# Kernel tuning notes

Measured on AMD Instinct MI355X. Metric: run time of the kernel, lower is better.

## Reference

```python
import jax, jax.numpy as jnp
import numpy as np

L, B, T = 512, 256, 128  # seq_length, batch_size, num_tags


def setup_inputs() -> dict:
    key = jax.random.key(0)
    k0, k1, k2, k3, k4 = jax.random.split(key, 5)
    emissions = jax.random.normal(k0, (L, B, T), dtype=jnp.float32)
    tags = jax.random.randint(k1, (L, B), 0, T)
    mask = jnp.ones((L, B), dtype=jnp.int32)
    # params per reset_parameters: uniform(-0.1, 0.1)
    start_transitions = jax.random.uniform(k2, (T,), jnp.float32, -0.1, 0.1)
    end_transitions = jax.random.uniform(k3, (T,), jnp.float32, -0.1, 0.1)
    transitions = jax.random.uniform(k4, (T, T), jnp.float32, -0.1, 0.1)
    return {
        'emissions': emissions,
        'tags': tags,
        'mask': mask,
        'start_transitions': start_transitions,
        'end_transitions': end_transitions,
        'transitions': transitions,
    }


def _compute_score(emissions, tags, maskf, start_transitions, end_transitions, transitions):
    # emissions: (L,B,T), tags/maskf: (L,B)
    # emission score at the gold tag for every (masked) position. The original
    # loop adds emissions[i][tags[i]]*mask[i] for i<L-1 and the last valid
    # position's emission via the end term; with 0/1 mask this equals the
    # full masked sum (padded positions contribute 0, last valid position is
    # counted exactly once either way).
    em_score = jnp.take_along_axis(emissions, tags[..., None], axis=2)[..., 0]  # (L,B)
    score = start_transitions[tags[0]] + jnp.sum(em_score * maskf, axis=0)  # (B,)
    # transition score between consecutive gold tags, masked by next position
    tr = transitions[tags[:-1], tags[1:]]  # (L-1,B)
    score = score + jnp.sum(tr * maskf[1:], axis=0)
    # end transition from the last valid tag of each sequence
    last_idx = jnp.sum(maskf, axis=0).astype(jnp.int32) - 1  # (B,)
    last_tags = jnp.take_along_axis(tags, last_idx[None, :], axis=0)[0]  # (B,)
    score = score + end_transitions[last_tags]
    return score


def _compute_normalizer(emissions, maskf, start_transitions, end_transitions, transitions):
    # forward algorithm: logsumexp recursion over timesteps via lax.scan
    def step(log_prob, xs):
        em, m = xs  # em: (B,T), m: (B,)
        # (B,T_prev,1) + (1,T_prev,T_next) + (B,1,T_next) -> logsumexp over prev
        score = jax.nn.logsumexp(
            log_prob[:, :, None] + transitions[None, :, :] + em[:, None, :], axis=1)
        log_prob = score * m[:, None] + log_prob * (1.0 - m[:, None])
        return log_prob, None

    lp0 = start_transitions[None, :] + emissions[0]  # (B,T)
    lp, _ = jax.lax.scan(jax.checkpoint(step), lp0, (emissions[1:], maskf[1:]))
    return jax.nn.logsumexp(lp + end_transitions[None, :], axis=1)  # (B,)


def reference(emissions, tags, mask, start_transitions, end_transitions, transitions):
    maskf = mask.astype(emissions.dtype)
    numerator = _compute_score(emissions, tags, maskf, start_transitions,
                               end_transitions, transitions)
    denominator = _compute_normalizer(emissions, maskf, start_transitions,
                                      end_transitions, transitions)
    llh = numerator - denominator  # (B,)
    return jnp.sum(llh)  # reduce=True (default)
```

## Files before the change

kernel.cpp:

```cpp
#include <hip/hip_runtime.h>

static constexpr int Lc = 512;
static constexpr int Bc = 256;
static constexpr int Tc = 128;

typedef _Float16 half2_t  __attribute__((ext_vector_type(2)));
typedef __fp16   fp16x2_t __attribute__((ext_vector_type(2)));

__device__ __forceinline__ float fdot2(half2_t a, half2_t b, float c) {
  return __builtin_amdgcn_fdot2(a, b, c, false);
}
__device__ __forceinline__ unsigned pack_h2(float a, float b) {
  union { fp16x2_t h; unsigned u; } cv;
  cv.h = __builtin_amdgcn_cvt_pkrtz(a, b);
  return cv.u;
}
__device__ __forceinline__ half2_t as_h2(unsigned u) {
  union { unsigned u; half2_t h; } cv;
  cv.u = u;
  return cv.h;
}
__device__ __forceinline__ float pair_add(float x) {
  const int y = __builtin_amdgcn_update_dpp(0, __float_as_int(x), 0xB1, 0xf, 0xf, true);
  return x + __int_as_float(y);
}
__device__ __forceinline__ float quad_fetch2(float x) {
  const int y = __builtin_amdgcn_update_dpp(0, __float_as_int(x), 0x4E, 0xf, 0xf, true);
  return __int_as_float(y);
}

__launch_bounds__(256, 1)
__global__ void crf_llh_kernel(const float* __restrict__ emis,
                               const int* __restrict__ tags,
                               const int* __restrict__ mask,
                               const float* __restrict__ startT,
                               const float* __restrict__ endT,
                               const float* __restrict__ trans,
                               float* __restrict__ pbuf,
                               float* __restrict__ qbuf,
                               float* __restrict__ meta)
{
  const int bid = blockIdx.x;
  const bool fwd = bid < Bc;
  const int b    = fwd ? bid : bid - Bc;
  const int tid  = threadIdx.x;
  const int j    = tid >> 1;
  const int h    = tid & 1;
  const int wid  = tid >> 6;
  const int lane = tid & 63;

  __shared__ __align__(16) unsigned p_lds[2][64];
  __shared__ int expo_lds[2];
  __shared__ float wredA[4];
  __shared__ float wredB[4];

  const size_t strideT = (size_t)Bc * Tc;
  const float* emp = emis + (size_t)b * Tc + j;

  if (fwd) {
    float score = 0.0f;
    {
      float v = 0.f, c = 0.f;
      #pragma unroll
      for (int s2 = 0; s2 < 2; ++s2) {
        const int t     = tid + s2 * 256;
        const float mf  = (float)mask[t * Bc + b];
        const int tag_t = tags[t * Bc + b];
        float e = emis[((size_t)t * Bc + b) * Tc + tag_t] * mf;
        if (t >= 1) e += trans[tags[(t - 1) * Bc + b] * Tc + tag_t] * mf;
        v += e; c += mf;
      }
      #pragma unroll
      for (int o = 1; o < 64; o <<= 1) {
        v += __shfl_xor(v, o);
        c += __shfl_xor(c, o);
      }
      if (lane == 0) { wredA[wid] = v; wredB[wid] = c; }
      __syncthreads();
      if (tid == 0) {
        const float sv = (wredA[0] + wredA[1]) + (wredA[2] + wredA[3]);
        const float sc = (wredB[0] + wredB[1]) + (wredB[2] + wredB[3]);
        const int last_idx = (int)(sc + 0.5f) - 1;
        score = sv + startT[tags[b]] + endT[tags[last_idx * Bc + b]];
      }
      __syncthreads();
    }

    unsigned Eu[32];
    #pragma unroll
    for (int q = 0; q < 32; ++q) {
      const float e0 = __expf(trans[(h * 64 + 2 * q)     * Tc + j]);
      const float e1 = __expf(trans[(h * 64 + 2 * q + 1) * Tc + j]);
      Eu[q] = pack_h2(e0, e1);
    }

    const float lp0 = startT[j] + emp[0];
    float wm = lp0;
    #pragma unroll
    for (int o = 1; o < 64; o <<= 1) wm = fmaxf(wm, __shfl_xor(wm, o));
    if (lane == 0) wredA[wid] = wm;
    __syncthreads();
    const float M0 = fmaxf(fmaxf(wredA[0], wredA[1]), fmaxf(wredA[2], wredA[3]));

    float pj = __expf(lp0 - M0);
    {
      const float partner = quad_fetch2(pj);
      if ((tid & 3) == 0) p_lds[0][tid >> 2] = pack_h2(pj, partner);
      if (tid == 0) expo_lds[0] = 0;
    }

    float emR0 = emp[1 * strideT], emR1 = emp[2 * strideT], emR2 = emp[3 * strideT];
    int   mR0  = mask[1 * Bc + b], mR1 = mask[2 * Bc + b], mR2 = mask[3 * Bc + b];
    const float* emp3 = emp + 4 * strideT;
    const int*   mp3  = mask + 4 * Bc + b;
    __syncthreads();

    int Ksum = 0, buf = 0;
    #pragma unroll 2
    for (int t = 1; t <= 255; ++t) {
      const int e0 = expo_lds[buf];
      const uint4* pv = (const uint4*)&p_lds[buf][h * 32];
      float a0 = 0.f, a1 = 0.f, a2 = 0.f, a3 = 0.f;
      float a4 = 0.f, a5 = 0.f, a6 = 0.f, a7 = 0.f;
      #pragma unroll
      for (int q = 0; q < 8; ++q) {
        const uint4 pq = pv[q];
        if (q & 1) {
          a4 = fdot2(as_h2(pq.x), as_h2(Eu[q * 4 + 0]), a4);
          a5 = fdot2(as_h2(pq.y), as_h2(Eu[q * 4 + 1]), a5);
          a6 = fdot2(as_h2(pq.z), as_h2(Eu[q * 4 + 2]), a6);
          a7 = fdot2(as_h2(pq.w), as_h2(Eu[q * 4 + 3]), a7);
        } else {
          a0 = fdot2(as_h2(pq.x), as_h2(Eu[q * 4 + 0]), a0);
          a1 = fdot2(as_h2(pq.y), as_h2(Eu[q * 4 + 1]), a1);
          a2 = fdot2(as_h2(pq.z), as_h2(Eu[q * 4 + 2]), a2);
          a3 = fdot2(as_h2(pq.w), as_h2(Eu[q * 4 + 3]), a3);
        }
      }
      float s = ((a0 + a1) + (a2 + a3)) + ((a4 + a5) + (a6 + a7));
      s = pair_add(s);

      const float eEm = __expf(emR0);
      const float emNew = emp3[0];
      const int   mNew  = mp3[0];
      emp3 += strideT; mp3 += Bc;

      const float r  = __uint_as_float((unsigned)(127 - e0) << 23);
      const float pn = (mR0 ? s * eEm : pj) * r;
      Ksum += e0;
      pj = pn;

      const int nxt = buf ^ 1;
      const float partner = quad_fetch2(pn);
      if ((tid & 3) == 0) p_lds[nxt][tid >> 2] = pack_h2(pn, partner);
      if (tid == 0) {
        int e = (int)((__float_as_uint(pn) >> 23) & 0xff) - 127;
        expo_lds[nxt] = min(max(e, -100), 100);
      }

      emR0 = emR1; emR1 = emR2; emR2 = emNew;
      mR0  = mR1;  mR1  = mR2;  mR2  = mNew;

      asm volatile("s_waitcnt lgkmcnt(0)" ::: "memory");
      __builtin_amdgcn_s_barrier();
      asm volatile("" ::: "memory");
      buf = nxt;
    }

    if (h == 0) pbuf[b * Tc + j] = pj;
    if (tid == 0) {
      meta[4 * b + 0] = score;
      meta[4 * b + 1] = M0;
      meta[4 * b + 2] = (float)Ksum;
    }
  } else {
    unsigned Eu[32];
    #pragma unroll
    for (int q = 0; q < 32; ++q) {
      const float2 tr2 = *(const float2*)&trans[j * Tc + h * 64 + 2 * q];
      Eu[q] = pack_h2(__expf(tr2.x), __expf(tr2.y));
    }

    float qi = __expf(endT[j]);
    {
      const float u = qi * __expf(emp[511 * strideT]);
      const float partner = quad_fetch2(u);
      if ((tid & 3) == 0) p_lds[0][tid >> 2] = pack_h2(u, partner);
      if (tid == 0) expo_lds[0] = 0;
    }

    int   mR0 = mask[511 * Bc + b], mR1 = mask[510 * Bc + b], mR2 = mask[509 * Bc + b];
    float emR0 = emp[510 * strideT], emR1 = emp[509 * strideT], emR2 = emp[508 * strideT];
    const float* emp3 = emp + 507 * strideT;
    const int*   mp3  = mask + 508 * Bc + b;
    __syncthreads();

    int Ksum = 0, buf = 0;
    #pragma unroll 2
    for (int k = 0; k < 256; ++k) {
      const int e0 = expo_lds[buf];
      const uint4* pv = (const uint4*)&p_lds[buf][h * 32];
      float a0 = 0.f, a1 = 0.f, a2 = 0.f, a3 = 0.f;
      float a4 = 0.f, a5 = 0.f, a6 = 0.f, a7 = 0.f;
      #pragma unroll
      for (int q = 0; q < 8; ++q) {
        const uint4 pq = pv[q];
        if (q & 1) {
          a4 = fdot2(as_h2(pq.x), as_h2(Eu[q * 4 + 0]), a4);
          a5 = fdot2(as_h2(pq.y), as_h2(Eu[q * 4 + 1]), a5);
          a6 = fdot2(as_h2(pq.z), as_h2(Eu[q * 4 + 2]), a6);
          a7 = fdot2(as_h2(pq.w), as_h2(Eu[q * 4 + 3]), a7);
        } else {
          a0 = fdot2(as_h2(pq.x), as_h2(Eu[q * 4 + 0]), a0);
          a1 = fdot2(as_h2(pq.y), as_h2(Eu[q * 4 + 1]), a1);
          a2 = fdot2(as_h2(pq.z), as_h2(Eu[q * 4 + 2]), a2);
          a3 = fdot2(as_h2(pq.w), as_h2(Eu[q * 4 + 3]), a3);
        }
      }
      float s = ((a0 + a1) + (a2 + a3)) + ((a4 + a5) + (a6 + a7));
      s = pair_add(s);

      const float emNew = emp3[0];
      const int   mNew  = mp3[0];
      emp3 -= strideT; mp3 -= Bc;

      const float r  = __uint_as_float((unsigned)(127 - e0) << 23);
      const float pn = (mR0 ? s : qi) * r;
      Ksum += e0;
      qi = pn;

      const int nxt = buf ^ 1;
      const float u = pn * __expf(emR0);
      const float partner = quad_fetch2(u);
      if ((tid & 3) == 0) p_lds[nxt][tid >> 2] = pack_h2(u, partner);
      if (tid == 0) {
        int e = (int)((__float_as_uint(pn) >> 23) & 0xff) - 127;
        expo_lds[nxt] = min(max(e, -100), 100);
      }

      mR0  = mR1;  mR1  = mR2;  mR2  = mNew;
      emR0 = emR1; emR1 = emR2; emR2 = emNew;

      asm volatile("s_waitcnt lgkmcnt(0)" ::: "memory");
      __builtin_amdgcn_s_barrier();
      asm volatile("" ::: "memory");
      buf = nxt;
    }

    if (h == 0) qbuf[b * Tc + j] = qi;
    if (tid == 0) meta[4 * b + 3] = (float)Ksum;
  }
}

__global__ void crf_meet(const float* __restrict__ pbuf,
                         const float* __restrict__ qbuf,
                         const float* __restrict__ meta,
                         float* __restrict__ partial)
{
  const int b = blockIdx.x;
  const int l = threadIdx.x;
  const float2 pp = *(const float2*)&pbuf[b * Tc + 2 * l];
  const float2 qq = *(const float2*)&qbuf[b * Tc + 2 * l];
  float d = pp.x * qq.x + pp.y * qq.y;
  #pragma unroll
  for (int o = 1; o < 64; o <<= 1) d += __shfl_xor(d, o);
  if (l == 0) {
    const float score = meta[4 * b + 0];
    const float M0    = meta[4 * b + 1];
    const float Ks    = meta[4 * b + 2] + meta[4 * b + 3];
    partial[b] = score - (M0 + Ks * 0.69314718055994531f + __logf(d));
  }
}

__global__ void crf_reduce(const float* __restrict__ partial, float* __restrict__ out)
{
  const int tid = threadIdx.x;
  float v = partial[tid];
  #pragma unroll
  for (int o = 1; o < 64; o <<= 1) v += __shfl_xor(v, o);
  __shared__ float ws[4];
  if ((tid & 63) == 0) ws[tid >> 6] = v;
  __syncthreads();
  if (tid == 0) out[0] = (ws[0] + ws[1]) + (ws[2] + ws[3]);
}

extern "C" void kernel_launch(void* const* d_in, const int* in_sizes, int n_in,
                              void* d_out, int out_size, void* d_ws, size_t ws_size,
                              hipStream_t stream)
{
  const float* emis   = (const float*)d_in[0];
  const int*   tags   = (const int*)d_in[1];
  const int*   mask   = (const int*)d_in[2];
  const float* startT = (const float*)d_in[3];
  const float* endT   = (const float*)d_in[4];
  const float* trans  = (const float*)d_in[5];

  float* ws      = (float*)d_ws;
  float* pbuf    = ws;
  float* qbuf    = ws + 32768;
  float* meta    = ws + 65536;
  float* partial = ws + 66560;

  crf_llh_kernel<<<2 * Bc, 256, 0, stream>>>(emis, tags, mask, startT, endT,
                                             trans, pbuf, qbuf, meta);
  crf_meet<<<Bc, 64, 0, stream>>>(pbuf, qbuf, meta, partial);
  crf_reduce<<<1, Bc, 0, stream>>>(partial, (float*)d_out);
}
```

Baseline: 122.0 us.

## Move gold-path score to meet kernel, shorten prefetch, raise loop priority

The gold-path numerator computation, with its gathers, reductions and two block barriers, moves out of the forward-chain blocks and into the meet kernel, which now runs 256 threads per batch. This shortens the critical sequential chain in the main kernel. The emission and mask prefetch depth drops from three steps ahead to two, which saves registers. s_setprio is raised around the recurrence body so that waves sharing a CU get scheduled ahead during the latency-critical part.

```diff
diff --git a/kernel.cpp b/kernel.cpp
--- a/kernel.cpp
+++ b/kernel.cpp
@@ -30,94 +30,65 @@
 }
 
 __launch_bounds__(256, 1)
-__global__ void crf_llh_kernel(const float* __restrict__ emis,
-                               const int* __restrict__ tags,
-                               const int* __restrict__ mask,
-                               const float* __restrict__ startT,
-                               const float* __restrict__ endT,
-                               const float* __restrict__ trans,
-                               float* __restrict__ pbuf,
-                               float* __restrict__ qbuf,
-                               float* __restrict__ meta)
+__global__ void crf_chain(const float* __restrict__ emis,
+                          const int* __restrict__ mask,
+                          const float* __restrict__ startT,
+                          const float* __restrict__ endT,
+                          const float* __restrict__ trans,
+                          float* __restrict__ pbuf,
+                          float* __restrict__ qbuf,
+                          float* __restrict__ meta)
 {
-  const int bid = blockIdx.x;
+  const int bid  = blockIdx.x;
   const bool fwd = bid < Bc;
   const int b    = fwd ? bid : bid - Bc;
   const int tid  = threadIdx.x;
-  const int j    = tid >> 1;
+  const int jj   = tid >> 1;
   const int h    = tid & 1;
   const int wid  = tid >> 6;
   const int lane = tid & 63;
 
   __shared__ __align__(16) unsigned p_lds[2][64];
   __shared__ int expo_lds[2];
-  __shared__ float wredA[4];
-  __shared__ float wredB[4];
+  __shared__ float wredM[4];
 
   const size_t strideT = (size_t)Bc * Tc;
-  const float* emp = emis + (size_t)b * Tc + j;
+  const float* emp = emis + (size_t)b * Tc + jj;
 
   if (fwd) {
-    float score = 0.0f;
-    {
-      float v = 0.f, c = 0.f;
-      #pragma unroll
-      for (int s2 = 0; s2 < 2; ++s2) {
-        const int t     = tid + s2 * 256;
-        const float mf  = (float)mask[t * Bc + b];
-        const int tag_t = tags[t * Bc + b];
-        float e = emis[((size_t)t * Bc + b) * Tc + tag_t] * mf;
-        if (t >= 1) e += trans[tags[(t - 1) * Bc + b] * Tc + tag_t] * mf;
-        v += e; c += mf;
-      }
-      #pragma unroll
-      for (int o = 1; o < 64; o <<= 1) {
-        v += __shfl_xor(v, o);
-        c += __shfl_xor(c, o);
-      }
-      if (lane == 0) { wredA[wid] = v; wredB[wid] = c; }
-      __syncthreads();
-      if (tid == 0) {
-        const float sv = (wredA[0] + wredA[1]) + (wredA[2] + wredA[3]);
-        const float sc = (wredB[0] + wredB[1]) + (wredB[2] + wredB[3]);
-        const int last_idx = (int)(sc + 0.5f) - 1;
-        score = sv + startT[tags[b]] + endT[tags[last_idx * Bc + b]];
-      }
-      __syncthreads();
-    }
-
     unsigned Eu[32];
     #pragma unroll
     for (int q = 0; q < 32; ++q) {
-      const float e0 = __expf(trans[(h * 64 + 2 * q)     * Tc + j]);
-      const float e1 = __expf(trans[(h * 64 + 2 * q + 1) * Tc + j]);
+      const float e0 = __expf(trans[(h * 64 + 2 * q)     * Tc + jj]);
+      const float e1 = __expf(trans[(h * 64 + 2 * q + 1) * Tc + jj]);
       Eu[q] = pack_h2(e0, e1);
     }
 
-    const float lp0 = startT[j] + emp[0];
+    const float lp0 = startT[jj] + emp[0];
     float wm = lp0;
     #pragma unroll
     for (int o = 1; o < 64; o <<= 1) wm = fmaxf(wm, __shfl_xor(wm, o));
-    if (lane == 0) wredA[wid] = wm;
+    if (lane == 0) wredM[wid] = wm;
     __syncthreads();
-    const float M0 = fmaxf(fmaxf(wredA[0], wredA[1]), fmaxf(wredA[2], wredA[3]));
-
-    float pj = __expf(lp0 - M0);
+    const float M0 = fmaxf(fmaxf(wredM[0], wredM[1]), fmaxf(wredM[2], wredM[3]));
+
+    float st = __expf(lp0 - M0);
     {
-      const float partner = quad_fetch2(pj);
-      if ((tid & 3) == 0) p_lds[0][tid >> 2] = pack_h2(pj, partner);
+      const float partner = quad_fetch2(st);
+      if ((tid & 3) == 0) p_lds[0][tid >> 2] = pack_h2(st, partner);
       if (tid == 0) expo_lds[0] = 0;
     }
 
-    float emR0 = emp[1 * strideT], emR1 = emp[2 * strideT], emR2 = emp[3 * strideT];
-    int   mR0  = mask[1 * Bc + b], mR1 = mask[2 * Bc + b], mR2 = mask[3 * Bc + b];
-    const float* emp3 = emp + 4 * strideT;
-    const int*   mp3  = mask + 4 * Bc + b;
+    float emR0 = emp[1 * strideT], emR1 = emp[2 * strideT];
+    int   mR0  = mask[1 * Bc + b], mR1 = mask[2 * Bc + b];
+    const float* emP = emp + 3 * strideT;
+    const int*   mP  = mask + 3 * Bc + b;
     __syncthreads();
 
-    int Ksum = 0, buf = 0;
+    int Ks = 0, buf = 0;
     #pragma unroll 2
     for (int t = 1; t <= 255; ++t) {
+      __builtin_amdgcn_s_setprio(1);
       const int e0 = expo_lds[buf];
       const uint4* pv = (const uint4*)&p_lds[buf][h * 32];
       float a0 = 0.f, a1 = 0.f, a2 = 0.f, a3 = 0.f;
@@ -141,14 +112,14 @@
       s = pair_add(s);
 
       const float eEm = __expf(emR0);
-      const float emNew = emp3[0];
-      const int   mNew  = mp3[0];
-      emp3 += strideT; mp3 += Bc;
+      const float emNew = emP[0];
+      const int   mNew  = mP[0];
+      emP += strideT; mP += Bc;
 
       const float r  = __uint_as_float((unsigned)(127 - e0) << 23);
-      const float pn = (mR0 ? s * eEm : pj) * r;
-      Ksum += e0;
-      pj = pn;
+      const float pn = (mR0 ? s * eEm : st) * r;
+      Ks += e0;
+      st = pn;
 
       const int nxt = buf ^ 1;
       const float partner = quad_fetch2(pn);
@@ -157,9 +128,10 @@
         int e = (int)((__float_as_uint(pn) >> 23) & 0xff) - 127;
         expo_lds[nxt] = min(max(e, -100), 100);
       }
-
-      emR0 = emR1; emR1 = emR2; emR2 = emNew;
-      mR0  = mR1;  mR1  = mR2;  mR2  = mNew;
+      __builtin_amdgcn_s_setprio(0);
+
+      emR0 = emR1; emR1 = emNew;
+      mR0  = mR1;  mR1  = mNew;
 
       asm volatile("s_waitcnt lgkmcnt(0)" ::: "memory");
       __builtin_amdgcn_s_barrier();
@@ -167,37 +139,37 @@
       buf = nxt;
     }
 
-    if (h == 0) pbuf[b * Tc + j] = pj;
+    if (h == 0) pbuf[b * Tc + jj] = st;
     if (tid == 0) {
-      meta[4 * b + 0] = score;
       meta[4 * b + 1] = M0;
-      meta[4 * b + 2] = (float)Ksum;
+      meta[4 * b + 2] = (float)Ks;
     }
   } else {
     unsigned Eu[32];
     #pragma unroll
     for (int q = 0; q < 32; ++q) {
-      const float2 tr2 = *(const float2*)&trans[j * Tc + h * 64 + 2 * q];
+      const float2 tr2 = *(const float2*)&trans[jj * Tc + h * 64 + 2 * q];
       Eu[q] = pack_h2(__expf(tr2.x), __expf(tr2.y));
     }
 
-    float qi = __expf(endT[j]);
+    float st = __expf(endT[jj]);
     {
-      const float u = qi * __expf(emp[511 * strideT]);
+      const float u = st * __expf(emp[511 * strideT]);
       const float partner = quad_fetch2(u);
       if ((tid & 3) == 0) p_lds[0][tid >> 2] = pack_h2(u, partner);
       if (tid == 0) expo_lds[0] = 0;
     }
 
-    int   mR0 = mask[511 * Bc + b], mR1 = mask[510 * Bc + b], mR2 = mask[509 * Bc + b];
-    float emR0 = emp[510 * strideT], emR1 = emp[509 * strideT], emR2 = emp[508 * strideT];
-    const float* emp3 = emp + 507 * strideT;
-    const int*   mp3  = mask + 508 * Bc + b;
+    int   mR0 = mask[511 * Bc + b], mR1 = mask[510 * Bc + b];
+    float emR0 = emp[510 * strideT], emR1 = emp[509 * strideT];
+    const float* emP = emp + 508 * strideT;
+    const int*   mP  = mask + 509 * Bc + b;
     __syncthreads();
 
-    int Ksum = 0, buf = 0;
+    int Ks = 0, buf = 0;
     #pragma unroll 2
     for (int k = 0; k < 256; ++k) {
+      __builtin_amdgcn_s_setprio(1);
       const int e0 = expo_lds[buf];
       const uint4* pv = (const uint4*)&p_lds[buf][h * 32];
       float a0 = 0.f, a1 = 0.f, a2 = 0.f, a3 = 0.f;
@@ -220,14 +192,14 @@
       float s = ((a0 + a1) + (a2 + a3)) + ((a4 + a5) + (a6 + a7));
       s = pair_add(s);
 
-      const float emNew = emp3[0];
-      const int   mNew  = mp3[0];
-      emp3 -= strideT; mp3 -= Bc;
+      const float emNew = emP[0];
+      const int   mNew  = mP[0];
+      emP -= strideT; mP -= Bc;
 
       const float r  = __uint_as_float((unsigned)(127 - e0) << 23);
-      const float pn = (mR0 ? s : qi) * r;
-      Ksum += e0;
-      qi = pn;
+      const float pn = (mR0 ? s : st) * r;
+      Ks += e0;
+      st = pn;
 
       const int nxt = buf ^ 1;
       const float u = pn * __expf(emR0);
@@ -237,9 +209,10 @@
         int e = (int)((__float_as_uint(pn) >> 23) & 0xff) - 127;
         expo_lds[nxt] = min(max(e, -100), 100);
       }
-
-      mR0  = mR1;  mR1  = mR2;  mR2  = mNew;
-      emR0 = emR1; emR1 = emR2; emR2 = emNew;
+      __builtin_amdgcn_s_setprio(0);
+
+      mR0  = mR1;  mR1  = mNew;
+      emR0 = emR1; emR1 = emNew;
 
       asm volatile("s_waitcnt lgkmcnt(0)" ::: "memory");
       __builtin_amdgcn_s_barrier();
@@ -247,28 +220,63 @@
       buf = nxt;
     }
 
-    if (h == 0) qbuf[b * Tc + j] = qi;
-    if (tid == 0) meta[4 * b + 3] = (float)Ksum;
+    if (h == 0) qbuf[b * Tc + jj] = st;
+    if (tid == 0) meta[4 * b + 3] = (float)Ks;
   }
 }
 
-__global__ void crf_meet(const float* __restrict__ pbuf,
+__global__ void crf_meet(const float* __restrict__ emis,
+                         const int* __restrict__ tags,
+                         const int* __restrict__ mask,
+                         const float* __restrict__ startT,
+                         const float* __restrict__ endT,
+                         const float* __restrict__ trans,
+                         const float* __restrict__ pbuf,
                          const float* __restrict__ qbuf,
                          const float* __restrict__ meta,
                          float* __restrict__ partial)
 {
-  const int b = blockIdx.x;
-  const int l = threadIdx.x;
-  const float2 pp = *(const float2*)&pbuf[b * Tc + 2 * l];
-  const float2 qq = *(const float2*)&qbuf[b * Tc + 2 * l];
-  float d = pp.x * qq.x + pp.y * qq.y;
+  const int b    = blockIdx.x;
+  const int tid  = threadIdx.x;
+  const int wid  = tid >> 6;
+  const int lane = tid & 63;
+
+  __shared__ float wredA[4];
+  __shared__ float wredB[4];
+
+  float v = 0.f, c = 0.f;
   #pragma unroll
-  for (int o = 1; o < 64; o <<= 1) d += __shfl_xor(d, o);
-  if (l == 0) {
-    const float score = meta[4 * b + 0];
-    const float M0    = meta[4 * b + 1];
-    const float Ks    = meta[4 * b + 2] + meta[4 * b + 3];
-    partial[b] = score - (M0 + Ks * 0.69314718055994531f + __logf(d));
+  for (int s2 = 0; s2 < 2; ++s2) {
+    const int t     = tid + s2 * 256;
+    const float mf  = (float)mask[t * Bc + b];
+    const int tag_t = tags[t * Bc + b];
+    float e = emis[((size_t)t * Bc + b) * Tc + tag_t] * mf;
+    if (t >= 1) e += trans[tags[(t - 1) * Bc + b] * Tc + tag_t] * mf;
+    v += e; c += mf;
+  }
+  #pragma unroll
+  for (int o = 1; o < 64; o <<= 1) {
+    v += __shfl_xor(v, o);
+    c += __shfl_xor(c, o);
+  }
+  if (lane == 0) { wredA[wid] = v; wredB[wid] = c; }
+  __syncthreads();
+
+  if (wid == 0) {
+    const float2 pp = *(const float2*)&pbuf[b * Tc + 2 * lane];
+    const float2 qq = *(const float2*)&qbuf[b * Tc + 2 * lane];
+    float d = pp.x * qq.x + pp.y * qq.y;
+    #pragma unroll
+    for (int o = 1; o < 64; o <<= 1) d += __shfl_xor(d, o);
+    if (lane == 0) {
+      const float sv = (wredA[0] + wredA[1]) + (wredA[2] + wredA[3]);
+      const float sc = (wredB[0] + wredB[1]) + (wredB[2] + wredB[3]);
+      const int last_idx = (int)(sc + 0.5f) - 1;
+      const float score = sv + startT[tags[b]] + endT[tags[last_idx * Bc + b]];
+      const float M0 = meta[4 * b + 1];
+      const float Ks = meta[4 * b + 2] + meta[4 * b + 3];
+      partial[b] = score - (M0 + Ks * 0.69314718055994531f + __logf(d));
+    }
   }
 }
 
@@ -301,8 +309,9 @@
   float* meta    = ws + 65536;
   float* partial = ws + 66560;
 
-  crf_llh_kernel<<<2 * Bc, 256, 0, stream>>>(emis, tags, mask, startT, endT,
-                                             trans, pbuf, qbuf, meta);
-  crf_meet<<<Bc, 64, 0, stream>>>(pbuf, qbuf, meta, partial);
+  crf_chain<<<2 * Bc, 256, 0, stream>>>(emis, mask, startT, endT, trans,
+                                        pbuf, qbuf, meta);
+  crf_meet<<<Bc, 256, 0, stream>>>(emis, tags, mask, startT, endT, trans,
+                                   pbuf, qbuf, meta, partial);
   crf_reduce<<<1, Bc, 0, stream>>>(partial, (float*)d_out);
 }
```

New measurement: 126.1 us. 3.3% more time.
